# Performance work log

Measured on AMD Instinct MI355X. Metric: run time of the kernel, lower is better.

The kernel has to match this reference:

```python
import jax, jax.numpy as jnp
from jax import lax
import numpy as np

B, H, W, C, N = 4, 512, 512, 32, 300000
K, S, P, D = 3, 2, 1, 1  # kernel, stride, padding, dilation


def setup_inputs() -> dict:
    key = jax.random.key(0)
    kf, _ = jax.random.split(key)
    features = jax.random.normal(kf, (N, C), dtype=jnp.float32)
    # unique active coordinates (spconv requires unique sites)
    rng = np.random.default_rng(0)
    lin = rng.choice(B * H * W, size=N, replace=False)
    b = lin // (H * W)
    y = (lin // W) % H
    x = lin % W
    coors = jnp.asarray(np.stack([b, y, x], axis=1), dtype=jnp.int32)  # [N,3]
    return {"features": features, "coors": coors, "batch_size": B}


def reference(features, coors, batch_size):
    # Scatter active features onto a dense grid initialized to -inf so that
    # inputs only; outputs with no active input in window are inactive).
    neg_inf = jnp.array(-jnp.inf, dtype=features.dtype)
    dense = jnp.full((batch_size, H, W, features.shape[1]), neg_inf,
                     dtype=features.dtype)
    b, y, x = coors[:, 0], coors[:, 1], coors[:, 2]
    dense = dense.at[b, y, x].set(features)  # coords are unique
    out = lax.reduce_window(
        dense, neg_inf, lax.max,
        window_dimensions=(1, K, K, 1),
        window_strides=(1, S, S, 1),
        padding=((0, 0), (P, P), (P, P), (0, 0)),
        window_dilation=(1, D, D, 1))
    # inactive output sites -> 0 (dense view of the sparse output tensor)
    return jnp.where(jnp.isinf(out), jnp.zeros((), out.dtype), out)
```

## Files before the change

kernel.cpp:

```cpp
#include <hip/hip_runtime.h>
#include <math.h>

#define BB 4
#define HH 512
#define WW 512
#define CC 32
#define HO 256
#define WO 256

#define ROWS 9
#define COLS 65
#define CELLS (ROWS * COLS)
#define OYPB 4

#define MAXOCC 256
#define OVFCAP 330

__global__ void scatter_idx_kernel(const int* __restrict__ coors,
                                   int* __restrict__ grid, int n) {
    int i = blockIdx.x * blockDim.x + threadIdx.x;
    if (i >= n) return;
    int b = coors[i * 3 + 0];
    int y = coors[i * 3 + 1];
    int x = coors[i * 3 + 2];
    grid[((size_t)b * HH + y) * WW + x] = i + 1;
}

__global__ void __launch_bounds__(256, 4)
pool_kernel(const float4* __restrict__ feat,
            const int* __restrict__ grid,
            float4* __restrict__ out,
            int npts) {
    int ox_base = (blockIdx.x & 7) * 32;
    int oy_base = ((blockIdx.x >> 3) & 63) * OYPB;
    int b       = blockIdx.x >> 9;

    int tid  = threadIdx.x;
    int lane = tid & 63;
    int cg   = tid & 7;
    int p    = tid >> 3;

    int iy0 = 2 * oy_base - 1;
    int gx0 = 2 * ox_base - 1;
    const int* gb = grid + (size_t)b * (HH * WW);

    __shared__ int    cnt;
    __shared__ int    smap[CELLS];
    __shared__ int    srcidx[MAXOCC];
    __shared__ float4 sfeat[MAXOCC * 8];
    __shared__ int    ovf_c[OVFCAP];
    __shared__ int    ovf_i[OVFCAP];

    const float NEG = -INFINITY;
    if (tid == 0) cnt = 0;
    if (tid < 8) sfeat[tid] = make_float4(NEG, NEG, NEG, NEG);
    __syncthreads();

    for (int cell = tid; cell < CELLS; cell += 256) {
        int v = 0;
        int r = cell / COLS;
        int c = cell - r * COLS;
        int iy = iy0 + r;
        int gx = gx0 + c;
        if ((unsigned)iy < (unsigned)HH && (unsigned)gx < (unsigned)WW) {
            int g = gb[iy * WW + gx];
            if ((unsigned)(g - 1) < (unsigned)npts) v = g;
        }
        unsigned long long mask = __ballot(v != 0);
        int nz = (int)__popcll(mask);
        int base = 0;
        if (lane == 0 && nz) base = atomicAdd(&cnt, nz);
        base = __shfl(base, 0);
        int s = 1 + base + (int)__popcll(mask & ((1ull << lane) - 1ull));
        int m = 0;
        if (v != 0) {
            if (s < MAXOCC) { srcidx[s] = v - 1; m = s; }
            else {
                int o = s - MAXOCC;
                ovf_c[o] = cell;
                ovf_i[o] = v - 1;
            }
        }
        smap[cell] = m;
    }
    __syncthreads();

    int hi = cnt < (MAXOCC - 1) ? cnt : (MAXOCC - 1);
    for (int s = 1 + (tid >> 3); s <= hi; s += 32)
        sfeat[(s << 3) + ((cg + s) & 7)] = feat[(size_t)srcidx[s] * 8 + cg];
    __syncthreads();

    int lc = 2 * p;
    bool ovf = (cnt >= MAXOCC);
    int novf = 0;
    if (ovf) {
        novf = cnt - (MAXOCC - 1);
        if (novf > OVFCAP) novf = OVFCAP;
    }

#pragma unroll
    for (int oyl = 0; oyl < OYPB; ++oyl) {
        float4 acc = make_float4(NEG, NEG, NEG, NEG);
#pragma unroll
        for (int dr = 0; dr < 3; ++dr) {
            int r = 2 * oyl + dr;
            int m0 = smap[r * COLS + lc + 0];
            int m1 = smap[r * COLS + lc + 1];
            int m2 = smap[r * COLS + lc + 2];
            float4 f0 = sfeat[(m0 << 3) + ((cg + m0) & 7)];
            float4 f1 = sfeat[(m1 << 3) + ((cg + m1) & 7)];
            float4 f2 = sfeat[(m2 << 3) + ((cg + m2) & 7)];
            acc.x = fmaxf(fmaxf(acc.x, f0.x), fmaxf(f1.x, f2.x));
            acc.y = fmaxf(fmaxf(acc.y, f0.y), fmaxf(f1.y, f2.y));
            acc.z = fmaxf(fmaxf(acc.z, f0.z), fmaxf(f1.z, f2.z));
            acc.w = fmaxf(fmaxf(acc.w, f0.w), fmaxf(f1.w, f2.w));
        }

        if (ovf) {
            for (int o = 0; o < novf; ++o) {
                int cell = ovf_c[o];
                int r = cell / COLS;
                int c = cell - r * COLS;
                if (c >= lc && c <= lc + 2 &&
                    r >= 2 * oyl && r <= 2 * oyl + 2) {
                    float4 fv = feat[(size_t)ovf_i[o] * 8 + cg];
                    acc.x = fmaxf(acc.x, fv.x);
                    acc.y = fmaxf(acc.y, fv.y);
                    acc.z = fmaxf(acc.z, fv.z);
                    acc.w = fmaxf(acc.w, fv.w);
                }
            }
        }

        acc.x = isinf(acc.x) ? 0.0f : acc.x;
        acc.y = isinf(acc.y) ? 0.0f : acc.y;
        acc.z = isinf(acc.z) ? 0.0f : acc.z;
        acc.w = isinf(acc.w) ? 0.0f : acc.w;

        size_t pos = ((size_t)(b * HO + oy_base + oyl) * WO + ox_base + p);
        out[pos * 8 + cg] = acc;
    }
}

extern "C" void kernel_launch(void* const* d_in, const int* in_sizes, int n_in,
                              void* d_out, int out_size, void* d_ws, size_t ws_size,
                              hipStream_t stream) {
    const float* features = (const float*)d_in[0];
    const int*   coors    = (const int*)d_in[1];
    int n = in_sizes[0] / CC;

    int* grid = (int*)d_ws;

    {
        int blk = 256, grd = (n + blk - 1) / blk;
        scatter_idx_kernel<<<grd, blk, 0, stream>>>(coors, grid, n);
    }
    {
        int grd = BB * (HO / OYPB) * (WO / 32);
        pool_kernel<<<grd, 256, 0, stream>>>((const float4*)features, grid,
                                             (float4*)d_out, n);
    }
}
```

Before: 105.0 us.

## Halve output rows per block and share the middle row's column max

Each block now covers 2 output rows instead of 4 (a 5-row input tile), so LDS use per block drops and the launch bound targets 8 blocks per SM. The 3-column max of each input row is computed once and the shared middle row feeds both output accumulators, which removes duplicate LDS reads. The trade-off is a larger halo fraction: more grid cells are re-read across neighbouring blocks and twice as many blocks are launched.

```diff
diff --git a/kernel.cpp b/kernel.cpp
--- a/kernel.cpp
+++ b/kernel.cpp
@@ -8,13 +8,14 @@
 #define HO 256
 #define WO 256
 
-#define ROWS 9
+#define ROWS 5
 #define COLS 65
 #define CELLS (ROWS * COLS)
-#define OYPB 4
+#define OYPB 2
 
-#define MAXOCC 256
-#define OVFCAP 330
+#define MAXOCC 128
+#define OVFCAP 198
+
 
 __global__ void scatter_idx_kernel(const int* __restrict__ coors,
                                    int* __restrict__ grid, int n) {
@@ -26,14 +27,14 @@
     grid[((size_t)b * HH + y) * WW + x] = i + 1;
 }
 
-__global__ void __launch_bounds__(256, 4)
+__global__ void __launch_bounds__(256, 8)
 pool_kernel(const float4* __restrict__ feat,
             const int* __restrict__ grid,
             float4* __restrict__ out,
             int npts) {
     int ox_base = (blockIdx.x & 7) * 32;
-    int oy_base = ((blockIdx.x >> 3) & 63) * OYPB;
-    int b       = blockIdx.x >> 9;
+    int oy_base = ((blockIdx.x >> 3) & 127) * OYPB;
+    int b       = blockIdx.x >> 10;
 
     int tid  = threadIdx.x;
     int lane = tid & 63;
@@ -91,55 +92,71 @@
     __syncthreads();
 
     int lc = 2 * p;
-    bool ovf = (cnt >= MAXOCC);
-    int novf = 0;
-    if (ovf) {
-        novf = cnt - (MAXOCC - 1);
-        if (novf > OVFCAP) novf = OVFCAP;
+    float4 acc0 = make_float4(NEG, NEG, NEG, NEG);
+    float4 acc1 = make_float4(NEG, NEG, NEG, NEG);
+#pragma unroll
+    for (int r = 0; r < ROWS; ++r) {
+        int m0 = smap[r * COLS + lc + 0];
+        int m1 = smap[r * COLS + lc + 1];
+        int m2 = smap[r * COLS + lc + 2];
+        float4 f0 = sfeat[(m0 << 3) + ((cg + m0) & 7)];
+        float4 f1 = sfeat[(m1 << 3) + ((cg + m1) & 7)];
+        float4 f2 = sfeat[(m2 << 3) + ((cg + m2) & 7)];
+        float tx = fmaxf(f0.x, fmaxf(f1.x, f2.x));
+        float ty = fmaxf(f0.y, fmaxf(f1.y, f2.y));
+        float tz = fmaxf(f0.z, fmaxf(f1.z, f2.z));
+        float tw = fmaxf(f0.w, fmaxf(f1.w, f2.w));
+        if (r <= 2) {
+            acc0.x = fmaxf(acc0.x, tx);
+            acc0.y = fmaxf(acc0.y, ty);
+            acc0.z = fmaxf(acc0.z, tz);
+            acc0.w = fmaxf(acc0.w, tw);
+        }
+        if (r >= 2) {
+            acc1.x = fmaxf(acc1.x, tx);
+            acc1.y = fmaxf(acc1.y, ty);
+            acc1.z = fmaxf(acc1.z, tz);
+            acc1.w = fmaxf(acc1.w, tw);
+        }
     }
 
-#pragma unroll
-    for (int oyl = 0; oyl < OYPB; ++oyl) {
-        float4 acc = make_float4(NEG, NEG, NEG, NEG);
-#pragma unroll
-        for (int dr = 0; dr < 3; ++dr) {
-            int r = 2 * oyl + dr;
-            int m0 = smap[r * COLS + lc + 0];
-            int m1 = smap[r * COLS + lc + 1];
-            int m2 = smap[r * COLS + lc + 2];
-            float4 f0 = sfeat[(m0 << 3) + ((cg + m0) & 7)];
-            float4 f1 = sfeat[(m1 << 3) + ((cg + m1) & 7)];
-            float4 f2 = sfeat[(m2 << 3) + ((cg + m2) & 7)];
-            acc.x = fmaxf(fmaxf(acc.x, f0.x), fmaxf(f1.x, f2.x));
-            acc.y = fmaxf(fmaxf(acc.y, f0.y), fmaxf(f1.y, f2.y));
-            acc.z = fmaxf(fmaxf(acc.z, f0.z), fmaxf(f1.z, f2.z));
-            acc.w = fmaxf(fmaxf(acc.w, f0.w), fmaxf(f1.w, f2.w));
-        }
-
-        if (ovf) {
-            for (int o = 0; o < novf; ++o) {
-                int cell = ovf_c[o];
-                int r = cell / COLS;
-                int c = cell - r * COLS;
-                if (c >= lc && c <= lc + 2 &&
-                    r >= 2 * oyl && r <= 2 * oyl + 2) {
-                    float4 fv = feat[(size_t)ovf_i[o] * 8 + cg];
-                    acc.x = fmaxf(acc.x, fv.x);
-                    acc.y = fmaxf(acc.y, fv.y);
-                    acc.z = fmaxf(acc.z, fv.z);
-                    acc.w = fmaxf(acc.w, fv.w);
+    if (cnt >= MAXOCC) {
+        int novf = cnt - (MAXOCC - 1);
+        if (novf > OVFCAP) novf = OVFCAP;
+        for (int o = 0; o < novf; ++o) {
+            int cell = ovf_c[o];
+            int r = cell / COLS;
+            int c = cell - r * COLS;
+            if (c >= lc && c <= lc + 2) {
+                float4 fv = feat[(size_t)ovf_i[o] * 8 + cg];
+                if (r <= 2) {
+                    acc0.x = fmaxf(acc0.x, fv.x);
+                    acc0.y = fmaxf(acc0.y, fv.y);
+                    acc0.z = fmaxf(acc0.z, fv.z);
+                    acc0.w = fmaxf(acc0.w, fv.w);
+                }
+                if (r >= 2) {
+                    acc1.x = fmaxf(acc1.x, fv.x);
+                    acc1.y = fmaxf(acc1.y, fv.y);
+                    acc1.z = fmaxf(acc1.z, fv.z);
+                    acc1.w = fmaxf(acc1.w, fv.w);
                 }
             }
         }
+    }
 
-        acc.x = isinf(acc.x) ? 0.0f : acc.x;
-        acc.y = isinf(acc.y) ? 0.0f : acc.y;
-        acc.z = isinf(acc.z) ? 0.0f : acc.z;
-        acc.w = isinf(acc.w) ? 0.0f : acc.w;
+    acc0.x = isinf(acc0.x) ? 0.0f : acc0.x;
+    acc0.y = isinf(acc0.y) ? 0.0f : acc0.y;
+    acc0.z = isinf(acc0.z) ? 0.0f : acc0.z;
+    acc0.w = isinf(acc0.w) ? 0.0f : acc0.w;
+    acc1.x = isinf(acc1.x) ? 0.0f : acc1.x;
+    acc1.y = isinf(acc1.y) ? 0.0f : acc1.y;
+    acc1.z = isinf(acc1.z) ? 0.0f : acc1.z;
+    acc1.w = isinf(acc1.w) ? 0.0f : acc1.w;
 
-        size_t pos = ((size_t)(b * HO + oy_base + oyl) * WO + ox_base + p);
-        out[pos * 8 + cg] = acc;
-    }
+    size_t pos0 = ((size_t)(b * HO + oy_base) * WO + ox_base + p);
+    out[pos0 * 8 + cg] = acc0;
+    out[(pos0 + WO) * 8 + cg] = acc1;
 }
 
 extern "C" void kernel_launch(void* const* d_in, const int* in_sizes, int n_in,
```

Measured after the change: 99.95 us. -4.8%, faster.
